# Kernel optimization log

Measured on AMD Instinct MI355X. Metric: run time of the kernel, lower is better.

The kernel has to match this reference:

```python
import jax, jax.numpy as jnp
import numpy as np

B = 16384
P = 16          # max_pos
D = 64          # per_digit_dim
C = 32          # carry_dim
N_OPS = 2
H = 256         # hidden
IN_DIM = 2 * D + N_OPS + C  # 162


def setup_inputs() -> dict:
    key = jax.random.key(0)
    ks = jax.random.split(key, 8)
    s1 = 1.0 / np.sqrt(IN_DIM)
    s2 = 1.0 / np.sqrt(H)
    return {
        "bias_a": jax.random.normal(ks[0], (B, P * D), dtype=jnp.float32),
        "bias_b": jax.random.normal(ks[1], (B, P * D), dtype=jnp.float32),
        "op": jax.random.uniform(ks[2], (B, N_OPS), dtype=jnp.float32),
        "W1": jax.random.normal(ks[3], (IN_DIM, H), dtype=jnp.float32) * s1,
        "b1": jnp.zeros((H,), dtype=jnp.float32),
        "W2": jax.random.normal(ks[4], (H, H), dtype=jnp.float32) * s2,
        "b2": jnp.zeros((H,), dtype=jnp.float32),
        "W3": jax.random.normal(ks[5], (H, D + C), dtype=jnp.float32) * s2,
        "b3": jnp.zeros((D + C,), dtype=jnp.float32),
    }


def reference(bias_a, bias_b, op, W1, b1, W2, b2, W3, b3):
    # [B, P*D] -> [P, B, D] for scanning over digit slots (low -> high)
    a = bias_a.reshape(B, P, D).transpose(1, 0, 2)
    b = bias_b.reshape(B, P, D).transpose(1, 0, 2)

    def step(carry, ab):
        a_i, b_i = ab
        x = jnp.concatenate([a_i, b_i, op, carry], axis=-1)  # [B, IN_DIM]
        h = jax.nn.relu(x @ W1 + b1)
        h = jax.nn.relu(h @ W2 + b2)
        y = h @ W3 + b3                                      # [B, D+C]
        return y[:, D:], y[:, :D]

    carry0 = jnp.zeros((B, C), dtype=bias_a.dtype)
    _, outs = jax.lax.scan(step, carry0, (a, b))             # outs: [P, B, D]
    return outs.transpose(1, 0, 2).reshape(B, P * D)
```

## Files before the change

### kernel.cpp

```cpp
#include <hip/hip_runtime.h>


typedef __attribute__((ext_vector_type(8))) short bf16x8;
typedef __attribute__((ext_vector_type(4))) float f32x4;
typedef __attribute__((ext_vector_type(2))) unsigned int u32x2;
typedef __attribute__((ext_vector_type(4))) unsigned int u32x4;

#define LDS_XAB 0
#define LDS_XC  16384
#define LDS_H1  24576
#define LDS_H2  57344
#define LDS_W3  90112
#define LDS_TOTAL 139264

__device__ inline unsigned short f32_to_bf16(float f) {
  unsigned int u = __builtin_bit_cast(unsigned int, f);
  u += 0x7FFFu + ((u >> 16) & 1u);
  return (unsigned short)(u >> 16);
}

__device__ inline unsigned int cvt_pk_bf16(float lo, float hi) {
  unsigned int r;
  asm("v_cvt_pk_bf16_f32 %0, %1, %2" : "=v"(r) : "v"(lo), "v"(hi));
  return r;
}

__global__ void pack_weights_kernel(const float* __restrict__ W1,
                                    const float* __restrict__ W2,
                                    const float* __restrict__ W3,
                                    unsigned short* __restrict__ wp) {
  int idx = blockIdx.x * 256 + threadIdx.x;
  if (idx >= 139264) return;
  int j, lane, frag, nt, kk, k, n;
  float v = 0.0f;
  if (idx < 49152) {
    int e = idx;
    j = e & 7; lane = (e >> 3) & 63; frag = e >> 9;
    nt = frag % 16; kk = frag / 16;
    k = kk * 32 + ((lane >> 4) << 3) + j;
    n = nt * 16 + (lane & 15);
    int ksrc;
    if (k < 128)      ksrc = k;
    else if (k < 160) ksrc = 130 + (k - 128);
    else if (k < 162) ksrc = 128 + (k - 160);
    else              ksrc = -1;
    v = (ksrc >= 0) ? W1[ksrc * 256 + n] : 0.0f;
  } else if (idx < 114688) {
    int e = idx - 49152;
    j = e & 7; lane = (e >> 3) & 63; frag = e >> 9;
    nt = frag % 16; kk = frag / 16;
    k = kk * 32 + ((lane >> 4) << 3) + j;
    n = nt * 16 + (lane & 15);
    v = W2[k * 256 + n];
  } else {
    int e = idx - 114688;
    j = e & 7; lane = (e >> 3) & 63; frag = e >> 9;
    nt = frag % 6; kk = frag / 6;
    k = kk * 32 + ((lane >> 4) << 3) + j;
    n = nt * 16 + (lane & 15);
    v = W3[k * 96 + n];
  }
  wp[idx] = f32_to_bf16(v);
}

__global__ __launch_bounds__(512, 2) void scan_kernel(
    const float* __restrict__ Ain, const float* __restrict__ Bin,
    const float* __restrict__ Op,
    const float* __restrict__ b1, const float* __restrict__ b2,
    const float* __restrict__ b3,
    const unsigned short* __restrict__ wp,
    float* __restrict__ out) {
  extern __shared__ char lds[];

  const int tid  = threadIdx.x;
  const int wave = tid >> 6, lane = tid & 63;
  const int lcol = lane & 15;
  const int q    = lane >> 4;
  const int row0 = blockIdx.x * 64;
  const int mw = wave >> 1, ngg = wave & 1;

  bf16x8 w1f[12], w2f[16];
  {
    const char* wb = (const char*)wp;
    #pragma unroll
    for (int kk = 0; kk < 6; ++kk)
      #pragma unroll
      for (int n = 0; n < 2; ++n)
        w1f[kk*2+n] = *(const bf16x8*)(wb + (size_t)(kk*16 + wave*2 + n)*1024 + lane*16);
    const char* wb2 = wb + 98304;
    #pragma unroll
    for (int kk = 0; kk < 8; ++kk)
      #pragma unroll
      for (int n = 0; n < 2; ++n)
        w2f[kk*2+n] = *(const bf16x8*)(wb2 + (size_t)(kk*16 + wave*2 + n)*1024 + lane*16);
  }
  f32x4 b1i[2], b2i[2], b3i[3];
  #pragma unroll
  for (int n = 0; n < 2; ++n)
    #pragma unroll
    for (int i = 0; i < 4; ++i) {
      b1i[n][i] = b1[(wave*2+n)*16 + q*4 + i];
      b2i[n][i] = b2[(wave*2+n)*16 + q*4 + i];
    }
  #pragma unroll
  for (int j = 0; j < 3; ++j)
    #pragma unroll
    for (int i = 0; i < 4; ++i)
      b3i[j][i] = b3[(ngg*3+j)*16 + q*4 + i];

  {
    const char* w3src = (const char*)wp + 229376;
    #pragma unroll
    for (int i = 0; i < 6; ++i)
      *(u32x4*)(lds + LDS_W3 + (size_t)(tid + i*512)*16) =
          *(const u32x4*)(w3src + (size_t)(tid + i*512)*16);
  }
  for (int i = tid; i < 4096; i += 512) {
    int r = i >> 6, kx = i & 63;
    unsigned short v = 0;
    if (kx == 32 || kx == 33) v = f32_to_bf16(Op[(size_t)(row0 + r)*2 + (kx - 32)]);
    int chunk = kx >> 3, within = (kx & 7) * 2;
    *(unsigned short*)(lds + LDS_XC + r*128 + ((chunk ^ (r & 7)) << 4) + within) = v;
  }

  const int part = tid & 7;
  const int srow = tid >> 3;
  const float* srcp = (part < 4 ? Ain : Bin) + (size_t)(row0 + srow)*1024 + (part & 3)*16;
  float4 pf[4];

  {
    #pragma unroll
    for (int jj = 0; jj < 4; ++jj) pf[jj] = *(const float4*)(srcp + jj*4);
    unsigned int u[8];
    #pragma unroll
    for (int jj = 0; jj < 4; ++jj) {
      u[jj*2]   = cvt_pk_bf16(pf[jj].x, pf[jj].y);
      u[jj*2+1] = cvt_pk_bf16(pf[jj].z, pf[jj].w);
    }
    u32x4 t0 = {u[0],u[1],u[2],u[3]}, t1 = {u[4],u[5],u[6],u[7]};
    *(u32x4*)(lds + LDS_XAB + srow*256 + (((part*2)   ^ (srow & 15)) << 4)) = t0;
    *(u32x4*)(lds + LDS_XAB + srow*256 + (((part*2+1) ^ (srow & 15)) << 4)) = t1;
    #pragma unroll
    for (int jj = 0; jj < 4; ++jj) pf[jj] = *(const float4*)(srcp + 64 + jj*4);
  }
  __syncthreads();

  #pragma unroll 1
  for (int p = 0; p < 16; ++p) {
    {
      f32x4 acc[2][4];
      #pragma unroll
      for (int n = 0; n < 2; ++n)
        #pragma unroll
        for (int m = 0; m < 4; ++m) acc[n][m] = b1i[n];
      #pragma unroll
      for (int m = 0; m < 4; ++m) {
        const int r = m*16 + lcol;
        bf16x8 xf[6];
        #pragma unroll
        for (int kk = 0; kk < 4; ++kk)
          xf[kk] = *(const bf16x8*)(lds + LDS_XAB + r*256 + (((4*kk + q) ^ lcol) << 4));
        #pragma unroll
        for (int kk = 0; kk < 2; ++kk)
          xf[4+kk] = *(const bf16x8*)(lds + LDS_XC + r*128 + (((4*kk + q) ^ (lcol & 7)) << 4));
        __builtin_amdgcn_s_setprio(1);
        #pragma unroll
        for (int kk = 0; kk < 6; ++kk) {
          acc[0][m] = __builtin_amdgcn_mfma_f32_16x16x32_bf16(w1f[kk*2+0], xf[kk], acc[0][m], 0,0,0);
          acc[1][m] = __builtin_amdgcn_mfma_f32_16x16x32_bf16(w1f[kk*2+1], xf[kk], acc[1][m], 0,0,0);
        }
        __builtin_amdgcn_s_setprio(0);
      }
      #pragma unroll
      for (int n = 0; n < 2; ++n) {
        const int nbyte = (wave*2+n)*32 + q*8;
        const int chunk = nbyte >> 4, within = nbyte & 15;
        #pragma unroll
        for (int m = 0; m < 4; ++m) {
          const int r = m*16 + lcol;
          float v0 = fmaxf(acc[n][m][0], 0.f);
          float v1 = fmaxf(acc[n][m][1], 0.f);
          float v2 = fmaxf(acc[n][m][2], 0.f);
          float v3 = fmaxf(acc[n][m][3], 0.f);
          u32x2 t; t.x = cvt_pk_bf16(v0, v1); t.y = cvt_pk_bf16(v2, v3);
          *(u32x2*)(lds + LDS_H1 + r*512 + ((chunk ^ lcol) << 4) + within) = t;
        }
      }
    }
    __syncthreads();

    if (p < 15) {
      unsigned int u[8];
      #pragma unroll
      for (int jj = 0; jj < 4; ++jj) {
        u[jj*2]   = cvt_pk_bf16(pf[jj].x, pf[jj].y);
        u[jj*2+1] = cvt_pk_bf16(pf[jj].z, pf[jj].w);
      }
      u32x4 t0 = {u[0],u[1],u[2],u[3]}, t1 = {u[4],u[5],u[6],u[7]};
      *(u32x4*)(lds + LDS_XAB + srow*256 + (((part*2)   ^ (srow & 15)) << 4)) = t0;
      *(u32x4*)(lds + LDS_XAB + srow*256 + (((part*2+1) ^ (srow & 15)) << 4)) = t1;
      if (p < 14) {
        const float* s2 = srcp + (p+2)*64;
        #pragma unroll
        for (int jj = 0; jj < 4; ++jj) pf[jj] = *(const float4*)(s2 + jj*4);
      }
    }

    {
      f32x4 acc[2][4];
      #pragma unroll
      for (int n = 0; n < 2; ++n)
        #pragma unroll
        for (int m = 0; m < 4; ++m) acc[n][m] = b2i[n];
      #pragma unroll
      for (int m = 0; m < 4; ++m) {
        const int r = m*16 + lcol;
        bf16x8 hf[8];
        #pragma unroll
        for (int kk = 0; kk < 8; ++kk)
          hf[kk] = *(const bf16x8*)(lds + LDS_H1 + r*512 + (((4*kk + q) ^ lcol) << 4));
        __builtin_amdgcn_s_setprio(1);
        #pragma unroll
        for (int kk = 0; kk < 8; ++kk) {
          acc[0][m] = __builtin_amdgcn_mfma_f32_16x16x32_bf16(w2f[kk*2+0], hf[kk], acc[0][m], 0,0,0);
          acc[1][m] = __builtin_amdgcn_mfma_f32_16x16x32_bf16(w2f[kk*2+1], hf[kk], acc[1][m], 0,0,0);
        }
        __builtin_amdgcn_s_setprio(0);
      }
      #pragma unroll
      for (int n = 0; n < 2; ++n) {
        const int nbyte = (wave*2+n)*32 + q*8;
        const int chunk = nbyte >> 4, within = nbyte & 15;
        #pragma unroll
        for (int m = 0; m < 4; ++m) {
          const int r = m*16 + lcol;
          float v0 = fmaxf(acc[n][m][0], 0.f);
          float v1 = fmaxf(acc[n][m][1], 0.f);
          float v2 = fmaxf(acc[n][m][2], 0.f);
          float v3 = fmaxf(acc[n][m][3], 0.f);
          u32x2 t; t.x = cvt_pk_bf16(v0, v1); t.y = cvt_pk_bf16(v2, v3);
          *(u32x2*)(lds + LDS_H2 + r*512 + ((chunk ^ lcol) << 4) + within) = t;
        }
      }
    }
    __syncthreads();

    {
      f32x4 acc3[3] = {b3i[0], b3i[1], b3i[2]};
      const int r = mw*16 + lcol;
      #pragma unroll
      for (int kk = 0; kk < 8; ++kk) {
        bf16x8 hf = *(const bf16x8*)(lds + LDS_H2 + r*512 + (((4*kk + q) ^ lcol) << 4));
        #pragma unroll
        for (int j = 0; j < 3; ++j) {
          bf16x8 wf = *(const bf16x8*)(lds + LDS_W3 + (size_t)(kk*6 + ngg*3 + j)*1024 + lane*16);
          acc3[j] = __builtin_amdgcn_mfma_f32_16x16x32_bf16(wf, hf, acc3[j], 0,0,0);
        }
      }
      #pragma unroll
      for (int j = 0; j < 3; ++j) {
        const int nt = ngg*3 + j;
        if (nt < 4) {
          float4 o;
          o.x = acc3[j][0]; o.y = acc3[j][1]; o.z = acc3[j][2]; o.w = acc3[j][3];
          *(float4*)&out[(size_t)(row0 + r)*1024 + p*64 + nt*16 + q*4] = o;
        } else {
          const int kbyte = (nt-4)*32 + q*8;
          const int chunk = kbyte >> 4, within = kbyte & 15;
          u32x2 t;
          t.x = cvt_pk_bf16(acc3[j][0], acc3[j][1]);
          t.y = cvt_pk_bf16(acc3[j][2], acc3[j][3]);
          *(u32x2*)(lds + LDS_XC + r*128 + ((chunk ^ (r & 7)) << 4) + within) = t;
        }
      }
    }
    __syncthreads();
  }
}

extern "C" void kernel_launch(void* const* d_in, const int* in_sizes, int n_in,
                              void* d_out, int out_size, void* d_ws, size_t ws_size,
                              hipStream_t stream) {
  const float* bias_a = (const float*)d_in[0];
  const float* bias_b = (const float*)d_in[1];
  const float* op     = (const float*)d_in[2];
  const float* W1     = (const float*)d_in[3];
  const float* b1     = (const float*)d_in[4];
  const float* W2     = (const float*)d_in[5];
  const float* b2     = (const float*)d_in[6];
  const float* W3     = (const float*)d_in[7];
  const float* b3     = (const float*)d_in[8];
  float* out = (float*)d_out;
  unsigned short* wp = (unsigned short*)d_ws;

  hipFuncSetAttribute((const void*)scan_kernel,
                      hipFuncAttributeMaxDynamicSharedMemorySize, LDS_TOTAL);

  pack_weights_kernel<<<544, 256, 0, stream>>>(W1, W2, W3, wp);
  scan_kernel<<<256, 512, LDS_TOTAL, stream>>>(bias_a, bias_b, op, b1, b2, b3, wp, out);
}
```

Measured before the change: 80.07 us.

## Overlap layer-3 of previous step with carry-independent layer-1 MFMAs, cut barriers

Restructures the recurrent step so the carry-independent part of layer 1 (the a/b digit columns) for step p runs together with layer 3 of step p-1. Only the carry columns of layer 1 wait on the new carry, which removes one barrier per step and interleaves independent MFMA chains. Biases move from registers into LDS to free VGPRs. The next digit's global load is issued just before layer 2 instead of being prefetched two steps ahead, which frees registers but reduces how far ahead the load runs. Layer 3 for the final step is peeled out after the loop.

```diff
diff --git a/kernel.cpp b/kernel.cpp
--- a/kernel.cpp
+++ b/kernel.cpp
@@ -11,7 +11,12 @@
 #define LDS_H1  24576
 #define LDS_H2  57344
 #define LDS_W3  90112
-#define LDS_TOTAL 139264
+#define LDS_B1  139264
+#define LDS_B2  140288
+#define LDS_B3  141312
+#define LDS_TOTAL 141696
+
+#define MFMA16(wf_, xf_, c_) c_ = __builtin_amdgcn_mfma_f32_16x16x32_bf16(wf_, xf_, c_, 0,0,0)
 
 __device__ inline unsigned short f32_to_bf16(float f) {
   unsigned int u = __builtin_bit_cast(unsigned int, f);
@@ -94,19 +99,10 @@
       for (int n = 0; n < 2; ++n)
         w2f[kk*2+n] = *(const bf16x8*)(wb2 + (size_t)(kk*16 + wave*2 + n)*1024 + lane*16);
   }
-  f32x4 b1i[2], b2i[2], b3i[3];
-  #pragma unroll
-  for (int n = 0; n < 2; ++n)
-    #pragma unroll
-    for (int i = 0; i < 4; ++i) {
-      b1i[n][i] = b1[(wave*2+n)*16 + q*4 + i];
-      b2i[n][i] = b2[(wave*2+n)*16 + q*4 + i];
-    }
-  #pragma unroll
-  for (int j = 0; j < 3; ++j)
-    #pragma unroll
-    for (int i = 0; i < 4; ++i)
-      b3i[j][i] = b3[(ngg*3+j)*16 + q*4 + i];
+
+  if (tid < 256) ((float*)(lds + LDS_B1))[tid] = b1[tid];
+  else           ((float*)(lds + LDS_B2))[tid - 256] = b2[tid - 256];
+  if (tid < 96)  ((float*)(lds + LDS_B3))[tid] = b3[tid];
 
   {
     const char* w3src = (const char*)wp + 229376;
@@ -126,49 +122,114 @@
   const int part = tid & 7;
   const int srow = tid >> 3;
   const float* srcp = (part < 4 ? Ain : Bin) + (size_t)(row0 + srow)*1024 + (part & 3)*16;
-  float4 pf[4];
 
   {
-    #pragma unroll
-    for (int jj = 0; jj < 4; ++jj) pf[jj] = *(const float4*)(srcp + jj*4);
+    float4 pv[4];
+    #pragma unroll
+    for (int jj = 0; jj < 4; ++jj) pv[jj] = *(const float4*)(srcp + jj*4);
     unsigned int u[8];
     #pragma unroll
     for (int jj = 0; jj < 4; ++jj) {
-      u[jj*2]   = cvt_pk_bf16(pf[jj].x, pf[jj].y);
-      u[jj*2+1] = cvt_pk_bf16(pf[jj].z, pf[jj].w);
+      u[jj*2]   = cvt_pk_bf16(pv[jj].x, pv[jj].y);
+      u[jj*2+1] = cvt_pk_bf16(pv[jj].z, pv[jj].w);
     }
     u32x4 t0 = {u[0],u[1],u[2],u[3]}, t1 = {u[4],u[5],u[6],u[7]};
     *(u32x4*)(lds + LDS_XAB + srow*256 + (((part*2)   ^ (srow & 15)) << 4)) = t0;
     *(u32x4*)(lds + LDS_XAB + srow*256 + (((part*2+1) ^ (srow & 15)) << 4)) = t1;
-    #pragma unroll
-    for (int jj = 0; jj < 4; ++jj) pf[jj] = *(const float4*)(srcp + 64 + jj*4);
   }
   __syncthreads();
+
+  const int r3 = mw*16 + lcol;
 
   #pragma unroll 1
   for (int p = 0; p < 16; ++p) {
+    f32x4 acc[2][4];
     {
-      f32x4 acc[2][4];
-      #pragma unroll
-      for (int n = 0; n < 2; ++n)
-        #pragma unroll
-        for (int m = 0; m < 4; ++m) acc[n][m] = b1i[n];
+      f32x4 bA = *(const f32x4*)(lds + LDS_B1 + (((wave*2+0)*16 + q*4) << 2));
+      f32x4 bB = *(const f32x4*)(lds + LDS_B1 + (((wave*2+1)*16 + q*4) << 2));
+      #pragma unroll
+      for (int mi = 0; mi < 4; ++mi) { acc[0][mi] = bA; acc[1][mi] = bB; }
+    }
+    if (p == 0) {
       #pragma unroll
       for (int m = 0; m < 4; ++m) {
         const int r = m*16 + lcol;
-        bf16x8 xf[6];
+        bf16x8 xf[4];
         #pragma unroll
         for (int kk = 0; kk < 4; ++kk)
           xf[kk] = *(const bf16x8*)(lds + LDS_XAB + r*256 + (((4*kk + q) ^ lcol) << 4));
+        __builtin_amdgcn_s_setprio(1);
+        #pragma unroll
+        for (int kk = 0; kk < 4; ++kk) {
+          MFMA16(w1f[kk*2+0], xf[kk], acc[0][m]);
+          MFMA16(w1f[kk*2+1], xf[kk], acc[1][m]);
+        }
+        __builtin_amdgcn_s_setprio(0);
+      }
+    } else {
+      f32x4 acc3[3];
+      #pragma unroll
+      for (int j = 0; j < 3; ++j)
+        acc3[j] = *(const f32x4*)(lds + LDS_B3 + ((((ngg*3+j)*16) + q*4) << 2));
+      #pragma unroll
+      for (int s = 0; s < 4; ++s) {
+        const int r = s*16 + lcol;
+        bf16x8 xf[4];
+        #pragma unroll
+        for (int kk = 0; kk < 4; ++kk)
+          xf[kk] = *(const bf16x8*)(lds + LDS_XAB + r*256 + (((4*kk + q) ^ lcol) << 4));
+        bf16x8 hfa = *(const bf16x8*)(lds + LDS_H2 + r3*512 + (((4*(2*s)   + q) ^ lcol) << 4));
+        bf16x8 hfb = *(const bf16x8*)(lds + LDS_H2 + r3*512 + (((4*(2*s+1) + q) ^ lcol) << 4));
+        bf16x8 wfa[3], wfb[3];
+        #pragma unroll
+        for (int j = 0; j < 3; ++j) {
+          wfa[j] = *(const bf16x8*)(lds + LDS_W3 + (size_t)((2*s)*6   + ngg*3 + j)*1024 + lane*16);
+          wfb[j] = *(const bf16x8*)(lds + LDS_W3 + (size_t)((2*s+1)*6 + ngg*3 + j)*1024 + lane*16);
+        }
+        __builtin_amdgcn_s_setprio(1);
+        #pragma unroll
+        for (int kk = 0; kk < 4; ++kk) {
+          MFMA16(w1f[kk*2+0], xf[kk], acc[0][s]);
+          MFMA16(w1f[kk*2+1], xf[kk], acc[1][s]);
+        }
+        #pragma unroll
+        for (int j = 0; j < 3; ++j) MFMA16(wfa[j], hfa, acc3[j]);
+        #pragma unroll
+        for (int j = 0; j < 3; ++j) MFMA16(wfb[j], hfb, acc3[j]);
+        __builtin_amdgcn_s_setprio(0);
+      }
+      #pragma unroll
+      for (int j = 0; j < 3; ++j) {
+        const int nt = ngg*3 + j;
+        if (nt < 4) {
+          float4 o;
+          o.x = acc3[j][0]; o.y = acc3[j][1]; o.z = acc3[j][2]; o.w = acc3[j][3];
+          *(float4*)&out[(size_t)(row0 + r3)*1024 + (p-1)*64 + nt*16 + q*4] = o;
+        } else {
+          const int kbyte = (nt-4)*32 + q*8;
+          const int chunk = kbyte >> 4, within = kbyte & 15;
+          u32x2 t;
+          t.x = cvt_pk_bf16(acc3[j][0], acc3[j][1]);
+          t.y = cvt_pk_bf16(acc3[j][2], acc3[j][3]);
+          *(u32x2*)(lds + LDS_XC + r3*128 + ((chunk ^ (r3 & 7)) << 4) + within) = t;
+        }
+      }
+    }
+    __syncthreads();
+
+    {
+      #pragma unroll
+      for (int m = 0; m < 4; ++m) {
+        const int r = m*16 + lcol;
+        bf16x8 xc[2];
         #pragma unroll
         for (int kk = 0; kk < 2; ++kk)
-          xf[4+kk] = *(const bf16x8*)(lds + LDS_XC + r*128 + (((4*kk + q) ^ (lcol & 7)) << 4));
+          xc[kk] = *(const bf16x8*)(lds + LDS_XC + r*128 + (((4*kk + q) ^ (lcol & 7)) << 4));
         __builtin_amdgcn_s_setprio(1);
-        #pragma unroll
-        for (int kk = 0; kk < 6; ++kk) {
-          acc[0][m] = __builtin_amdgcn_mfma_f32_16x16x32_bf16(w1f[kk*2+0], xf[kk], acc[0][m], 0,0,0);
-          acc[1][m] = __builtin_amdgcn_mfma_f32_16x16x32_bf16(w1f[kk*2+1], xf[kk], acc[1][m], 0,0,0);
-        }
+        MFMA16(w1f[8],  xc[0], acc[0][m]);
+        MFMA16(w1f[9],  xc[0], acc[1][m]);
+        MFMA16(w1f[10], xc[1], acc[0][m]);
+        MFMA16(w1f[11], xc[1], acc[1][m]);
         __builtin_amdgcn_s_setprio(0);
       }
       #pragma unroll
@@ -189,29 +250,22 @@
     }
     __syncthreads();
 
-    if (p < 15) {
-      unsigned int u[8];
-      #pragma unroll
-      for (int jj = 0; jj < 4; ++jj) {
-        u[jj*2]   = cvt_pk_bf16(pf[jj].x, pf[jj].y);
-        u[jj*2+1] = cvt_pk_bf16(pf[jj].z, pf[jj].w);
-      }
-      u32x4 t0 = {u[0],u[1],u[2],u[3]}, t1 = {u[4],u[5],u[6],u[7]};
-      *(u32x4*)(lds + LDS_XAB + srow*256 + (((part*2)   ^ (srow & 15)) << 4)) = t0;
-      *(u32x4*)(lds + LDS_XAB + srow*256 + (((part*2+1) ^ (srow & 15)) << 4)) = t1;
-      if (p < 14) {
-        const float* s2 = srcp + (p+2)*64;
-        #pragma unroll
-        for (int jj = 0; jj < 4; ++jj) pf[jj] = *(const float4*)(s2 + jj*4);
-      }
-    }
-
     {
-      f32x4 acc[2][4];
-      #pragma unroll
-      for (int n = 0; n < 2; ++n)
-        #pragma unroll
-        for (int m = 0; m < 4; ++m) acc[n][m] = b2i[n];
+      float4 t0, t1, t2, t3;
+      if (p < 15) {
+        const float* s1 = srcp + (p+1)*64;
+        t0 = *(const float4*)(s1 + 0);
+        t1 = *(const float4*)(s1 + 4);
+        t2 = *(const float4*)(s1 + 8);
+        t3 = *(const float4*)(s1 + 12);
+      }
+      f32x4 acc2[2][4];
+      {
+        f32x4 bA = *(const f32x4*)(lds + LDS_B2 + (((wave*2+0)*16 + q*4) << 2));
+        f32x4 bB = *(const f32x4*)(lds + LDS_B2 + (((wave*2+1)*16 + q*4) << 2));
+        #pragma unroll
+        for (int mi = 0; mi < 4; ++mi) { acc2[0][mi] = bA; acc2[1][mi] = bB; }
+      }
       #pragma unroll
       for (int m = 0; m < 4; ++m) {
         const int r = m*16 + lcol;
@@ -222,8 +276,8 @@
         __builtin_amdgcn_s_setprio(1);
         #pragma unroll
         for (int kk = 0; kk < 8; ++kk) {
-          acc[0][m] = __builtin_amdgcn_mfma_f32_16x16x32_bf16(w2f[kk*2+0], hf[kk], acc[0][m], 0,0,0);
-          acc[1][m] = __builtin_amdgcn_mfma_f32_16x16x32_bf16(w2f[kk*2+1], hf[kk], acc[1][m], 0,0,0);
+          MFMA16(w2f[kk*2+0], hf[kk], acc2[0][m]);
+          MFMA16(w2f[kk*2+1], hf[kk], acc2[1][m]);
         }
         __builtin_amdgcn_s_setprio(0);
       }
@@ -234,47 +288,51 @@
         #pragma unroll
         for (int m = 0; m < 4; ++m) {
           const int r = m*16 + lcol;
-          float v0 = fmaxf(acc[n][m][0], 0.f);
-          float v1 = fmaxf(acc[n][m][1], 0.f);
-          float v2 = fmaxf(acc[n][m][2], 0.f);
-          float v3 = fmaxf(acc[n][m][3], 0.f);
+          float v0 = fmaxf(acc2[n][m][0], 0.f);
+          float v1 = fmaxf(acc2[n][m][1], 0.f);
+          float v2 = fmaxf(acc2[n][m][2], 0.f);
+          float v3 = fmaxf(acc2[n][m][3], 0.f);
           u32x2 t; t.x = cvt_pk_bf16(v0, v1); t.y = cvt_pk_bf16(v2, v3);
           *(u32x2*)(lds + LDS_H2 + r*512 + ((chunk ^ lcol) << 4) + within) = t;
         }
       }
+      if (p < 15) {
+        unsigned int u[8];
+        u[0] = cvt_pk_bf16(t0.x, t0.y);  u[1] = cvt_pk_bf16(t0.z, t0.w);
+        u[2] = cvt_pk_bf16(t1.x, t1.y);  u[3] = cvt_pk_bf16(t1.z, t1.w);
+        u[4] = cvt_pk_bf16(t2.x, t2.y);  u[5] = cvt_pk_bf16(t2.z, t2.w);
+        u[6] = cvt_pk_bf16(t3.x, t3.y);  u[7] = cvt_pk_bf16(t3.z, t3.w);
+        u32x4 w0 = {u[0],u[1],u[2],u[3]}, w1 = {u[4],u[5],u[6],u[7]};
+        *(u32x4*)(lds + LDS_XAB + srow*256 + (((part*2)   ^ (srow & 15)) << 4)) = w0;
+        *(u32x4*)(lds + LDS_XAB + srow*256 + (((part*2+1) ^ (srow & 15)) << 4)) = w1;
+      }
     }
     __syncthreads();
-
-    {
-      f32x4 acc3[3] = {b3i[0], b3i[1], b3i[2]};
-      const int r = mw*16 + lcol;
-      #pragma unroll
-      for (int kk = 0; kk < 8; ++kk) {
-        bf16x8 hf = *(const bf16x8*)(lds + LDS_H2 + r*512 + (((4*kk + q) ^ lcol) << 4));
-        #pragma unroll
-        for (int j = 0; j < 3; ++j) {
-          bf16x8 wf = *(const bf16x8*)(lds + LDS_W3 + (size_t)(kk*6 + ngg*3 + j)*1024 + lane*16);
-          acc3[j] = __builtin_amdgcn_mfma_f32_16x16x32_bf16(wf, hf, acc3[j], 0,0,0);
-        }
-      }
+  }
+
+  {
+    f32x4 acc3[3];
+    #pragma unroll
+    for (int j = 0; j < 3; ++j)
+      acc3[j] = *(const f32x4*)(lds + LDS_B3 + ((((ngg*3+j)*16) + q*4) << 2));
+    #pragma unroll
+    for (int kk = 0; kk < 8; ++kk) {
+      bf16x8 hf = *(const bf16x8*)(lds + LDS_H2 + r3*512 + (((4*kk + q) ^ lcol) << 4));
       #pragma unroll
       for (int j = 0; j < 3; ++j) {
-        const int nt = ngg*3 + j;
-        if (nt < 4) {
-          float4 o;
-          o.x = acc3[j][0]; o.y = acc3[j][1]; o.z = acc3[j][2]; o.w = acc3[j][3];
-          *(float4*)&out[(size_t)(row0 + r)*1024 + p*64 + nt*16 + q*4] = o;
-        } else {
-          const int kbyte = (nt-4)*32 + q*8;
-          const int chunk = kbyte >> 4, within = kbyte & 15;
-          u32x2 t;
-          t.x = cvt_pk_bf16(acc3[j][0], acc3[j][1]);
-          t.y = cvt_pk_bf16(acc3[j][2], acc3[j][3]);
-          *(u32x2*)(lds + LDS_XC + r*128 + ((chunk ^ (r & 7)) << 4) + within) = t;
-        }
-      }
-    }
-    __syncthreads();
+        bf16x8 wf = *(const bf16x8*)(lds + LDS_W3 + (size_t)(kk*6 + ngg*3 + j)*1024 + lane*16);
+        MFMA16(wf, hf, acc3[j]);
+      }
+    }
+    #pragma unroll
+    for (int j = 0; j < 3; ++j) {
+      const int nt = ngg*3 + j;
+      if (nt < 4) {
+        float4 o;
+        o.x = acc3[j][0]; o.y = acc3[j][1]; o.z = acc3[j][2]; o.w = acc3[j][3];
+        *(float4*)&out[(size_t)(row0 + r3)*1024 + 15*64 + nt*16 + q*4] = o;
+      }
+    }
   }
 }
 
```

Result: slower. 88.19 us (+10.1%).
